# Kernel tuning notes

Measured on AMD Instinct MI355X. Metric: run time of the kernel, lower is better.

The kernel has to match this reference:

```python
import jax, jax.numpy as jnp
import numpy as np
import math

H = 16
D_MODEL = 1024
D_K = D_MODEL // H


def setup_inputs() -> dict:
    key = jax.random.key(0)
    ks = jax.random.split(key, 11)
    B, S = 2, 2048
    scale = 1.0 / math.sqrt(D_MODEL)
    inp = {
        "query": jax.random.normal(ks[0], (B, S, D_MODEL), dtype=jnp.float32),
        "key": jax.random.normal(ks[1], (B, S, D_MODEL), dtype=jnp.float32),
        "value": jax.random.normal(ks[2], (B, S, D_MODEL), dtype=jnp.float32),
        # torch nn.Linear convention: W is [out_features, in_features]
        "Wq": jax.random.normal(ks[3], (D_MODEL, D_MODEL), dtype=jnp.float32) * scale,
        "bq": jnp.zeros((D_MODEL,), dtype=jnp.float32),
        "Wk": jax.random.normal(ks[4], (D_MODEL, D_MODEL), dtype=jnp.float32) * scale,
        "bk": jnp.zeros((D_MODEL,), dtype=jnp.float32),
        "Wv": jax.random.normal(ks[5], (D_MODEL, D_MODEL), dtype=jnp.float32) * scale,
        "bv": jnp.zeros((D_MODEL,), dtype=jnp.float32),
        "Wo": jax.random.normal(ks[6], (D_MODEL, D_MODEL), dtype=jnp.float32) * scale,
        "bo": jnp.zeros((D_MODEL,), dtype=jnp.float32),
    }
    return inp


def _split_heads(x):
    # [b, s, h*d_k] -> [b, h, s, d_k]
    b, s, _ = x.shape
    return x.reshape(b, s, H, D_K).transpose(0, 2, 1, 3)


def reference(query, key, value, Wq, bq, Wk, bk, Wv, bv, Wo, bo):
    q = _split_heads(query @ Wq.T + bq)
    k = _split_heads(key @ Wk.T + bk)
    v = _split_heads(value @ Wv.T + bv)
    # scaled dot-product attention, full L x L scores per head
    scores = jnp.einsum("bhqd,bhkd->bhqk", q, k) / math.sqrt(D_K)
    attn = jax.nn.softmax(scores, axis=-1)
    ctx = jnp.einsum("bhqk,bhkd->bhqd", attn, v)  # [b, h, s, d_k]
    b, h, s, d = ctx.shape
    ctx = ctx.transpose(0, 2, 1, 3).reshape(b, s, h * d)
    return ctx @ Wo.T + bo
```

## Files before the change

kernel.cpp:

```cpp
#include <hip/hip_runtime.h>

typedef unsigned int u32;
typedef unsigned short u16;
typedef __attribute__((ext_vector_type(8))) short short8;
typedef __attribute__((ext_vector_type(4))) float f32x4;
typedef __attribute__((ext_vector_type(2))) u32 u32x2;

#define DEV __device__ __forceinline__

DEV u16 f2bf(float f) {
  u32 u = __builtin_bit_cast(u32, f);
  u = (u + 0x7FFFu + ((u >> 16) & 1u)) >> 16;
  return (u16)u;
}

DEV float fexp2(float x) {
#if __has_builtin(__builtin_amdgcn_exp2f)
  return __builtin_amdgcn_exp2f(x);
#else
  return exp2f(x);
#endif
}

DEV u32 cvt_pk_bf16(float lo, float hi) {
  u32 r;
  asm("v_cvt_pk_bf16_f32 %0, %1, %2" : "=v"(r) : "v"(lo), "v"(hi));
  return r;
}

DEV void llds16(const void* g, void* lds) {
  __builtin_amdgcn_global_load_lds(
      (const __attribute__((address_space(1))) u32*)g,
      (__attribute__((address_space(3))) u32*)lds, 16, 0, 0);
}

struct CvtArgs {
  const float* src[7];
  u16* dst[7];
};

__global__ void cvt_all(CvtArgs ca) {
  int i = blockIdx.x * blockDim.x + threadIdx.x;
  int chunk = i >> 17;
  int seg = chunk < 12 ? (chunk >> 2) : (chunk - 9);
  u32 base8 = (seg < 3) ? (u32)seg * 524288u : 1572864u + ((u32)seg - 3) * 131072u;
  size_t off = ((size_t)i - base8) * 8;
  const f32x4* p = (const f32x4*)(ca.src[seg] + off);
  f32x4 a = p[0], b = p[1];
  short8 o;
  o[0] = (short)f2bf(a[0]); o[1] = (short)f2bf(a[1]);
  o[2] = (short)f2bf(a[2]); o[3] = (short)f2bf(a[3]);
  o[4] = (short)f2bf(b[0]); o[5] = (short)f2bf(b[1]);
  o[6] = (short)f2bf(b[2]); o[7] = (short)f2bf(b[3]);
  *(short8*)(ca.dst[seg] + off) = o;
}

struct GemmArgs {
  const u16* A[3];
  const u16* W[3];
  const float* bias[3];
  void* C[3];
  float scale[3];
};

template <int BM, int BN, int WAVES_M, int OUT_BF16>
__global__ __launch_bounds__(256, 2) void gemm_bt(GemmArgs ga) {
  constexpr int K = 1024, N = 1024;
  constexpr int WAVES_N = 4 / WAVES_M;
  constexpr int WM = BM / WAVES_M, WN = BN / WAVES_N;
  constexpr int AM = WM / 16, AN = WN / 16;
  constexpr int SEGS = (BM + BN) / 16;
  constexpr int PW = SEGS / 4;

  __shared__ u16 lsA[BM * 32];
  __shared__ u16 lsB[BN * 32];

  const int z = blockIdx.z;
  const u16* __restrict__ A = ga.A[z];
  const u16* __restrict__ W = ga.W[z];
  const int tid = threadIdx.x;
  const int l = tid & 63, w = tid >> 6;
  const int lg = l >> 4, lr = l & 15;
  const int bn = blockIdx.x, bm = blockIdx.y;
  const int wm = w / WAVES_N, wn = w % WAVES_N;

  f32x4 acc[AM][AN];
#pragma unroll
  for (int i = 0; i < AM; ++i)
#pragma unroll
    for (int j = 0; j < AN; ++j) acc[i][j] = (f32x4){0.f, 0.f, 0.f, 0.f};

  for (int k0 = 0; k0 < K; k0 += 32) {
    __syncthreads();
#pragma unroll
    for (int i = 0; i < PW; ++i) {
      int s = w * PW + i;
      if (s < BM / 16) {
        u32 sb = s * 1024;
        u32 lb = sb + l * 16;
        u32 row = lb >> 6, colS = (lb & 63) >> 1;
        llds16(A + (size_t)(bm * BM + row) * K + k0 + colS, (char*)lsA + sb);
      } else {
        u32 sb = (u32)(s - BM / 16) * 1024;
        u32 lb = sb + l * 16;
        u32 row = lb >> 6, colS = (lb & 63) >> 1;
        llds16(W + (size_t)(bn * BN + row) * K + k0 + colS, (char*)lsB + sb);
      }
    }
    __syncthreads();
    short8 af[AM], bf[AN];
#pragma unroll
    for (int i = 0; i < AM; ++i)
      af[i] = *(const short8*)&lsA[(wm * WM + i * 16 + lr) * 32 + lg * 8];
#pragma unroll
    for (int j = 0; j < AN; ++j)
      bf[j] = *(const short8*)&lsB[(wn * WN + j * 16 + lr) * 32 + lg * 8];
#pragma unroll
    for (int i = 0; i < AM; ++i)
#pragma unroll
      for (int j = 0; j < AN; ++j)
        acc[i][j] = __builtin_amdgcn_mfma_f32_16x16x32_bf16(af[i], bf[j], acc[i][j], 0, 0, 0);
  }

  const float sc = ga.scale[z];
  const float* __restrict__ bias = ga.bias[z];
#pragma unroll
  for (int j = 0; j < AN; ++j) {
    int col = bn * BN + wn * WN + j * 16 + lr;
    float bv = bias[col];
#pragma unroll
    for (int i = 0; i < AM; ++i) {
      int row0 = bm * BM + wm * WM + i * 16 + lg * 4;
#pragma unroll
      for (int r = 0; r < 4; ++r) {
        float v = (acc[i][j][r] + bv) * sc;
        if constexpr (OUT_BF16)
          ((u16*)ga.C[z])[(size_t)(row0 + r) * N + col] = f2bf(v);
        else
          ((float*)ga.C[z])[(size_t)(row0 + r) * N + col] = v;
      }
    }
  }
}

__global__ __launch_bounds__(256, 4) void attn_fwd(
    const u16* __restrict__ Q, const u16* __restrict__ Kp,
    const u16* __restrict__ V, u16* __restrict__ O) {
  constexpr int S = 2048, LD = 1024;
  __shared__ u16 Kt[2][64 * 64];
  __shared__ u16 Vt[2][64 * 64];
  __shared__ u16 Pl[4][16 * 64];
  const int tid = threadIdx.x;
  const int l = tid & 63, w = tid >> 6;
  const int lg = l >> 4, lr = l & 15;
  const int qt = blockIdx.x, h = blockIdx.y, b = blockIdx.z;
  const size_t base = ((size_t)b * S) * LD + h * 64;
  const int qrow = qt * 64 + w * 16 + lr;

  short8 qf[2];
#pragma unroll
  for (int c = 0; c < 2; ++c)
    qf[c] = *(const short8*)&Q[base + (size_t)qrow * LD + c * 32 + lg * 8];

  f32x4 acc[4];
#pragma unroll
  for (int i = 0; i < 4; ++i) acc[i] = (f32x4){0.f, 0.f, 0.f, 0.f};
  float lsum = 0.f;

  const int vkey = (tid & 31) * 2;
  const int vd0 = (tid >> 5) * 8;

  short8 va = *(const short8*)&V[base + (size_t)vkey * LD + vd0];
  short8 vb = *(const short8*)&V[base + (size_t)(vkey + 1) * LD + vd0];
#pragma unroll
  for (int i = 0; i < 2; ++i) {
    u32 sb = (u32)(w * 2048 + i * 1024);
    u32 lb = sb + l * 16;
    u32 key = lb >> 7;
    u32 inner = (lb & 127) ^ ((key & 7) << 4);
    llds16(Kp + base + (size_t)key * LD + (inner >> 1), (char*)Kt[0] + sb);
  }
#pragma unroll
  for (int jj = 0; jj < 8; ++jj) {
    u32 pv = (u32)(u16)va[jj] | ((u32)(u16)vb[jj] << 16);
    u32 addr = (u32)((vd0 + jj) * 128 + vkey * 2) ^ ((u32)jj << 4);
    *(u32*)((char*)Vt[0] + addr) = pv;
  }
  __syncthreads();

  int cur = 0;
  for (int t = 0; t < 32; ++t) {
    const int kb = t * 64;
    short8 nva, nvb;
    if (t < 31) {
      nva = *(const short8*)&V[base + (size_t)(kb + 64 + vkey) * LD + vd0];
      nvb = *(const short8*)&V[base + (size_t)(kb + 64 + vkey + 1) * LD + vd0];
#pragma unroll
      for (int i = 0; i < 2; ++i) {
        u32 sb = (u32)(w * 2048 + i * 1024);
        u32 lb = sb + l * 16;
        u32 key = lb >> 7;
        u32 inner = (lb & 127) ^ ((key & 7) << 4);
        llds16(Kp + base + (size_t)(kb + 64 + key) * LD + (inner >> 1),
               (char*)Kt[cur ^ 1] + sb);
      }
    }

    float p[16];
    __builtin_amdgcn_s_setprio(1);
#pragma unroll
    for (int ks = 0; ks < 4; ++ks) {
      f32x4 s = (f32x4){0.f, 0.f, 0.f, 0.f};
#pragma unroll
      for (int c = 0; c < 2; ++c) {
        u32 addr = (u32)((ks * 16 + lr) * 128 + c * 64 + lg * 16) ^ ((u32)(lr & 7) << 4);
        short8 kf = *(const short8*)((const char*)Kt[cur] + addr);
        s = __builtin_amdgcn_mfma_f32_16x16x32_bf16(kf, qf[c], s, 0, 0, 0);
      }
      p[ks * 4 + 0] = s[0]; p[ks * 4 + 1] = s[1];
      p[ks * 4 + 2] = s[2]; p[ks * 4 + 3] = s[3];
    }
    __builtin_amdgcn_s_setprio(0);
#pragma unroll
    for (int i = 0; i < 16; ++i) {
      float e = fexp2(p[i]);
      p[i] = e;
      lsum += e;
    }
#pragma unroll
    for (int ks = 0; ks < 4; ++ks) {
      u32 w0 = cvt_pk_bf16(p[ks * 4 + 0], p[ks * 4 + 1]);
      u32 w1 = cvt_pk_bf16(p[ks * 4 + 2], p[ks * 4 + 3]);
      u32 addr = (u32)(lr * 128 + (ks * 16 + lg * 4) * 2) ^ ((u32)(lr & 7) << 4);
      u32x2 pw = {w0, w1};
      *(u32x2*)((char*)&Pl[w][0] + addr) = pw;
    }
    __builtin_amdgcn_s_setprio(1);
#pragma unroll
    for (int ds = 0; ds < 4; ++ds) {
#pragma unroll
      for (int c = 0; c < 2; ++c) {
        u32 va_ = (u32)((ds * 16 + lr) * 128 + c * 64 + lg * 16) ^ ((u32)(lr & 7) << 4);
        short8 vf = *(const short8*)((const char*)Vt[cur] + va_);
        u32 pa_ = (u32)(lr * 128 + c * 64 + lg * 16) ^ ((u32)(lr & 7) << 4);
        short8 pf = *(const short8*)((const char*)&Pl[w][0] + pa_);
        acc[ds] = __builtin_amdgcn_mfma_f32_16x16x32_bf16(vf, pf, acc[ds], 0, 0, 0);
      }
    }
    __builtin_amdgcn_s_setprio(0);

    if (t < 31) {
#pragma unroll
      for (int jj = 0; jj < 8; ++jj) {
        u32 pv = (u32)(u16)nva[jj] | ((u32)(u16)nvb[jj] << 16);
        u32 addr = (u32)((vd0 + jj) * 128 + vkey * 2) ^ ((u32)jj << 4);
        *(u32*)((char*)Vt[cur ^ 1] + addr) = pv;
      }
    }
    __syncthreads();
    cur ^= 1;
  }

  lsum += __shfl_xor(lsum, 16);
  lsum += __shfl_xor(lsum, 32);
  float inv = __builtin_amdgcn_rcpf(lsum);
#pragma unroll
  for (int ds = 0; ds < 4; ++ds)
#pragma unroll
    for (int r = 0; r < 4; ++r)
      O[base + (size_t)qrow * LD + ds * 16 + lg * 4 + r] = f2bf(acc[ds][r] * inv);
}

extern "C" void kernel_launch(void* const* d_in, const int* in_sizes, int n_in,
                              void* d_out, int out_size, void* d_ws, size_t ws_size,
                              hipStream_t stream) {
  constexpr size_t SZ_X = 4096ull * 1024;
  constexpr size_t SZ_W = 1024ull * 1024;
  const float* bq = (const float*)d_in[4];
  const float* bk = (const float*)d_in[6];
  const float* bv = (const float*)d_in[8];
  const float* bo = (const float*)d_in[10];

  char* ws = (char*)d_ws;
  u16* xq = (u16*)ws;
  u16* xk = xq + SZ_X;
  u16* xv = xk + SZ_X;
  u16* wqb = xv + SZ_X;
  u16* wkb = wqb + SZ_W;
  u16* wvb = wkb + SZ_W;
  u16* wob = wvb + SZ_W;
  u16* Qp = wob + SZ_W;
  u16* Kp = Qp + SZ_X;
  u16* Vp = Kp + SZ_X;
  u16* Cx = Vp + SZ_X;

  CvtArgs ca;
  ca.src[0] = (const float*)d_in[0]; ca.dst[0] = xq;
  ca.src[1] = (const float*)d_in[1]; ca.dst[1] = xk;
  ca.src[2] = (const float*)d_in[2]; ca.dst[2] = xv;
  ca.src[3] = (const float*)d_in[3]; ca.dst[3] = wqb;
  ca.src[4] = (const float*)d_in[5]; ca.dst[4] = wkb;
  ca.src[5] = (const float*)d_in[7]; ca.dst[5] = wvb;
  ca.src[6] = (const float*)d_in[9]; ca.dst[6] = wob;
  cvt_all<<<dim3(8192), 256, 0, stream>>>(ca);

  GemmArgs g1;
  g1.A[0] = xq;  g1.A[1] = xk;  g1.A[2] = xv;
  g1.W[0] = wqb; g1.W[1] = wkb; g1.W[2] = wvb;
  g1.bias[0] = bq; g1.bias[1] = bk; g1.bias[2] = bv;
  g1.C[0] = Qp; g1.C[1] = Kp; g1.C[2] = Vp;
  g1.scale[0] = 0.18033688011112042f;
  g1.scale[1] = 1.f; g1.scale[2] = 1.f;
  gemm_bt<128, 128, 2, 1><<<dim3(8, 32, 3), 256, 0, stream>>>(g1);

  attn_fwd<<<dim3(32, 16, 2), 256, 0, stream>>>(Qp, Kp, Vp, Cx);

  GemmArgs g2 = {};
  g2.A[0] = Cx; g2.W[0] = wob; g2.bias[0] = bo; g2.C[0] = d_out; g2.scale[0] = 1.f;
  gemm_bt<64, 128, 1, 0><<<dim3(8, 64, 1), 256, 0, stream>>>(g2);
}
```

Before: 147.5 us.

## Process two query groups per wave and keep P in registers

The attention kernel now gives each wave 32 query rows instead of 16, so every K and V fragment read from LDS is reused across two MFMA groups, and each block covers 128 queries. The P matrix no longer goes through LDS: V keys are permuted via key0 so the bf16-packed exp values already sit in the MFMA B-operand layout. The output store is vectorised. The grid is halved and the launch bound drops to 2 blocks per SM, trading occupancy for more registers and less LDS traffic.

```diff
diff --git a/kernel.cpp b/kernel.cpp
--- a/kernel.cpp
+++ b/kernel.cpp
@@ -5,6 +5,7 @@
 typedef __attribute__((ext_vector_type(8))) short short8;
 typedef __attribute__((ext_vector_type(4))) float f32x4;
 typedef __attribute__((ext_vector_type(2))) u32 u32x2;
+typedef __attribute__((ext_vector_type(4))) u32 u32x4;
 
 #define DEV __device__ __forceinline__
 
@@ -143,48 +144,63 @@
   }
 }
 
-__global__ __launch_bounds__(256, 4) void attn_fwd(
+__global__ __launch_bounds__(256, 2) void attn_fwd(
     const u16* __restrict__ Q, const u16* __restrict__ Kp,
     const u16* __restrict__ V, u16* __restrict__ O) {
   constexpr int S = 2048, LD = 1024;
   __shared__ u16 Kt[2][64 * 64];
   __shared__ u16 Vt[2][64 * 64];
-  __shared__ u16 Pl[4][16 * 64];
   const int tid = threadIdx.x;
   const int l = tid & 63, w = tid >> 6;
   const int lg = l >> 4, lr = l & 15;
   const int qt = blockIdx.x, h = blockIdx.y, b = blockIdx.z;
   const size_t base = ((size_t)b * S) * LD + h * 64;
-  const int qrow = qt * 64 + w * 16 + lr;
-
-  short8 qf[2];
-#pragma unroll
-  for (int c = 0; c < 2; ++c)
-    qf[c] = *(const short8*)&Q[base + (size_t)qrow * LD + c * 32 + lg * 8];
-
-  f32x4 acc[4];
-#pragma unroll
-  for (int i = 0; i < 4; ++i) acc[i] = (f32x4){0.f, 0.f, 0.f, 0.f};
-  float lsum = 0.f;
-
-  const int vkey = (tid & 31) * 2;
+  const int q0 = qt * 128 + w * 32;
+
+  short8 qf[2][2];
+#pragma unroll
+  for (int g = 0; g < 2; ++g)
+#pragma unroll
+    for (int c = 0; c < 2; ++c)
+      qf[g][c] = *(const short8*)&Q[base + (size_t)(q0 + g * 16 + lr) * LD + c * 32 + lg * 8];
+
+  f32x4 acc[2][4];
+#pragma unroll
+  for (int g = 0; g < 2; ++g)
+#pragma unroll
+    for (int i = 0; i < 4; ++i) acc[g][i] = (f32x4){0.f, 0.f, 0.f, 0.f};
+  float lsum[2] = {0.f, 0.f};
+
+  const int m = tid & 31;
+  const int kp0 = m * 2;
+  const int key0 = ((m & 16) << 1) + ((m & 2) << 3) + (((m >> 2) & 3) << 2) + ((m & 1) << 1);
   const int vd0 = (tid >> 5) * 8;
 
-  short8 va = *(const short8*)&V[base + (size_t)vkey * LD + vd0];
-  short8 vb = *(const short8*)&V[base + (size_t)(vkey + 1) * LD + vd0];
-#pragma unroll
-  for (int i = 0; i < 2; ++i) {
-    u32 sb = (u32)(w * 2048 + i * 1024);
-    u32 lb = sb + l * 16;
-    u32 key = lb >> 7;
-    u32 inner = (lb & 127) ^ ((key & 7) << 4);
-    llds16(Kp + base + (size_t)key * LD + (inner >> 1), (char*)Kt[0] + sb);
-  }
-#pragma unroll
-  for (int jj = 0; jj < 8; ++jj) {
-    u32 pv = (u32)(u16)va[jj] | ((u32)(u16)vb[jj] << 16);
-    u32 addr = (u32)((vd0 + jj) * 128 + vkey * 2) ^ ((u32)jj << 4);
-    *(u32*)((char*)Vt[0] + addr) = pv;
+#define KSTAGE(T, BUF)                                                          \
+  {                                                                             \
+    _Pragma("unroll") for (int i_ = 0; i_ < 2; ++i_) {                          \
+      u32 sb = (u32)(w * 2 + i_) * 1024;                                        \
+      u32 lb = sb + l * 16;                                                     \
+      u32 key = lb >> 7;                                                        \
+      u32 inner = (lb & 127) ^ ((key & 7) << 4);                                \
+      llds16(Kp + base + (size_t)((T) * 64 + key) * LD + (inner >> 1),          \
+             (char*)Kt[BUF] + sb);                                              \
+    }                                                                           \
+  }
+#define VWRITE(BUF, VA, VB)                                                     \
+  {                                                                             \
+    _Pragma("unroll") for (int jj = 0; jj < 8; ++jj) {                          \
+      u32 pv = (u32)(u16)(VA)[jj] | ((u32)(u16)(VB)[jj] << 16);                 \
+      u32 addr = (u32)((vd0 + jj) * 128 + kp0 * 2) ^ ((u32)jj << 4);            \
+      *(u32*)((char*)Vt[BUF] + addr) = pv;                                      \
+    }                                                                           \
+  }
+
+  {
+    short8 va = *(const short8*)&V[base + (size_t)key0 * LD + vd0];
+    short8 vb = *(const short8*)&V[base + (size_t)(key0 + 1) * LD + vd0];
+    KSTAGE(0, 0);
+    VWRITE(0, va, vb);
   }
   __syncthreads();
 
@@ -193,82 +209,84 @@
     const int kb = t * 64;
     short8 nva, nvb;
     if (t < 31) {
-      nva = *(const short8*)&V[base + (size_t)(kb + 64 + vkey) * LD + vd0];
-      nvb = *(const short8*)&V[base + (size_t)(kb + 64 + vkey + 1) * LD + vd0];
-#pragma unroll
-      for (int i = 0; i < 2; ++i) {
-        u32 sb = (u32)(w * 2048 + i * 1024);
-        u32 lb = sb + l * 16;
-        u32 key = lb >> 7;
-        u32 inner = (lb & 127) ^ ((key & 7) << 4);
-        llds16(Kp + base + (size_t)(kb + 64 + key) * LD + (inner >> 1),
-               (char*)Kt[cur ^ 1] + sb);
-      }
-    }
-
-    float p[16];
+      nva = *(const short8*)&V[base + (size_t)(kb + 64 + key0) * LD + vd0];
+      nvb = *(const short8*)&V[base + (size_t)(kb + 64 + key0 + 1) * LD + vd0];
+      KSTAGE(t + 1, cur ^ 1);
+    }
+
+    f32x4 sv[2][4];
     __builtin_amdgcn_s_setprio(1);
 #pragma unroll
     for (int ks = 0; ks < 4; ++ks) {
-      f32x4 s = (f32x4){0.f, 0.f, 0.f, 0.f};
+      u32 a0 = (u32)(((ks * 16 + lr) * 128 + lg * 16) ^ ((lr & 7) << 4));
+      short8 kf0 = *(const short8*)((const char*)Kt[cur] + a0);
+      short8 kf1 = *(const short8*)((const char*)Kt[cur] + (a0 ^ 64));
+#pragma unroll
+      for (int g = 0; g < 2; ++g) {
+        f32x4 s = (f32x4){0.f, 0.f, 0.f, 0.f};
+        s = __builtin_amdgcn_mfma_f32_16x16x32_bf16(kf0, qf[g][0], s, 0, 0, 0);
+        s = __builtin_amdgcn_mfma_f32_16x16x32_bf16(kf1, qf[g][1], s, 0, 0, 0);
+        sv[g][ks] = s;
+      }
+    }
+    __builtin_amdgcn_s_setprio(0);
+
+    u32 pk[2][8];
+#pragma unroll
+    for (int g = 0; g < 2; ++g) {
+#pragma unroll
+      for (int ks = 0; ks < 4; ++ks) {
+#pragma unroll
+        for (int r = 0; r < 4; ++r) {
+          float e = fexp2(sv[g][ks][r]);
+          sv[g][ks][r] = e;
+          lsum[g] += e;
+        }
+        pk[g][ks * 2 + 0] = cvt_pk_bf16(sv[g][ks][0], sv[g][ks][1]);
+        pk[g][ks * 2 + 1] = cvt_pk_bf16(sv[g][ks][2], sv[g][ks][3]);
+      }
+    }
+
+    __builtin_amdgcn_s_setprio(1);
+#pragma unroll
+    for (int ds = 0; ds < 4; ++ds) {
 #pragma unroll
       for (int c = 0; c < 2; ++c) {
-        u32 addr = (u32)((ks * 16 + lr) * 128 + c * 64 + lg * 16) ^ ((u32)(lr & 7) << 4);
-        short8 kf = *(const short8*)((const char*)Kt[cur] + addr);
-        s = __builtin_amdgcn_mfma_f32_16x16x32_bf16(kf, qf[c], s, 0, 0, 0);
-      }
-      p[ks * 4 + 0] = s[0]; p[ks * 4 + 1] = s[1];
-      p[ks * 4 + 2] = s[2]; p[ks * 4 + 3] = s[3];
+        u32 va_ = (u32)(((ds * 16 + lr) * 128 + c * 64 + lg * 16) ^ ((lr & 7) << 4));
+        short8 vf = *(const short8*)((const char*)Vt[cur] + va_);
+#pragma unroll
+        for (int g = 0; g < 2; ++g) {
+          u32x4 pc = {pk[g][c * 4 + 0], pk[g][c * 4 + 1], pk[g][c * 4 + 2], pk[g][c * 4 + 3]};
+          short8 pf = __builtin_bit_cast(short8, pc);
+          acc[g][ds] = __builtin_amdgcn_mfma_f32_16x16x32_bf16(vf, pf, acc[g][ds], 0, 0, 0);
+        }
+      }
     }
     __builtin_amdgcn_s_setprio(0);
-#pragma unroll
-    for (int i = 0; i < 16; ++i) {
-      float e = fexp2(p[i]);
-      p[i] = e;
-      lsum += e;
-    }
-#pragma unroll
-    for (int ks = 0; ks < 4; ++ks) {
-      u32 w0 = cvt_pk_bf16(p[ks * 4 + 0], p[ks * 4 + 1]);
-      u32 w1 = cvt_pk_bf16(p[ks * 4 + 2], p[ks * 4 + 3]);
-      u32 addr = (u32)(lr * 128 + (ks * 16 + lg * 4) * 2) ^ ((u32)(lr & 7) << 4);
-      u32x2 pw = {w0, w1};
-      *(u32x2*)((char*)&Pl[w][0] + addr) = pw;
-    }
-    __builtin_amdgcn_s_setprio(1);
-#pragma unroll
-    for (int ds = 0; ds < 4; ++ds) {
-#pragma unroll
-      for (int c = 0; c < 2; ++c) {
-        u32 va_ = (u32)((ds * 16 + lr) * 128 + c * 64 + lg * 16) ^ ((u32)(lr & 7) << 4);
-        short8 vf = *(const short8*)((const char*)Vt[cur] + va_);
-        u32 pa_ = (u32)(lr * 128 + c * 64 + lg * 16) ^ ((u32)(lr & 7) << 4);
-        short8 pf = *(const short8*)((const char*)&Pl[w][0] + pa_);
-        acc[ds] = __builtin_amdgcn_mfma_f32_16x16x32_bf16(vf, pf, acc[ds], 0, 0, 0);
-      }
-    }
-    __builtin_amdgcn_s_setprio(0);
-
-    if (t < 31) {
-#pragma unroll
-      for (int jj = 0; jj < 8; ++jj) {
-        u32 pv = (u32)(u16)nva[jj] | ((u32)(u16)nvb[jj] << 16);
-        u32 addr = (u32)((vd0 + jj) * 128 + vkey * 2) ^ ((u32)jj << 4);
-        *(u32*)((char*)Vt[cur ^ 1] + addr) = pv;
-      }
-    }
+
+    if (t < 31) VWRITE(cur ^ 1, nva, nvb);
     __syncthreads();
     cur ^= 1;
   }
 
-  lsum += __shfl_xor(lsum, 16);
-  lsum += __shfl_xor(lsum, 32);
-  float inv = __builtin_amdgcn_rcpf(lsum);
-#pragma unroll
-  for (int ds = 0; ds < 4; ++ds)
-#pragma unroll
-    for (int r = 0; r < 4; ++r)
-      O[base + (size_t)qrow * LD + ds * 16 + lg * 4 + r] = f2bf(acc[ds][r] * inv);
+#pragma unroll
+  for (int g = 0; g < 2; ++g) {
+    lsum[g] += __shfl_xor(lsum[g], 16);
+    lsum[g] += __shfl_xor(lsum[g], 32);
+  }
+#pragma unroll
+  for (int g = 0; g < 2; ++g) {
+    float inv = __builtin_amdgcn_rcpf(lsum[g]);
+#pragma unroll
+    for (int ds = 0; ds < 4; ++ds) {
+      u32x2 ov;
+      ov[0] = cvt_pk_bf16(acc[g][ds][0] * inv, acc[g][ds][1] * inv);
+      ov[1] = cvt_pk_bf16(acc[g][ds][2] * inv, acc[g][ds][3] * inv);
+      *(u32x2*)&O[base + (size_t)(q0 + g * 16 + lr) * LD + ds * 16 + lg * 4] = ov;
+    }
+  }
+#undef KSTAGE
+#undef VWRITE
 }
 
 extern "C" void kernel_launch(void* const* d_in, const int* in_sizes, int n_in,
@@ -313,7 +331,7 @@
   g1.scale[1] = 1.f; g1.scale[2] = 1.f;
   gemm_bt<128, 128, 2, 1><<<dim3(8, 32, 3), 256, 0, stream>>>(g1);
 
-  attn_fwd<<<dim3(32, 16, 2), 256, 0, stream>>>(Qp, Kp, Vp, Cx);
+  attn_fwd<<<dim3(16, 16, 2), 256, 0, stream>>>(Qp, Kp, Vp, Cx);
 
   GemmArgs g2 = {};
   g2.A[0] = Cx; g2.W[0] = wob; g2.bias[0] = bo; g2.C[0] = d_out; g2.scale[0] = 1.f;
```

After: 140.2 us. 5.0% less time.
